# Performance work log

Hardware: AMD Instinct MI355X
Metric: run time of the kernel (lower is better)

The kernel has to match this reference:

```python
import jax, jax.numpy as jnp
import numpy as np

B, C, LQ, D = 4096, 64, 32, 128
H = 192  # 1.5 * dim
MARGIN = 1.0
EPS = 1e-12


def l2norm(x):
    return x * jax.lax.rsqrt(jnp.maximum(jnp.sum(x * x, axis=1, keepdims=True), EPS))


def setup_inputs() -> dict:
    key = jax.random.key(0)
    ks = jax.random.split(key, 16)
    question_word_embs = jax.random.normal(ks[0], (B, LQ, D), jnp.float32)
    question_lengths = jax.random.randint(ks[1], (B,), 1, LQ + 1, jnp.int32)
    header_embs = jax.random.normal(ks[2], (B, C, D), jnp.float32)
    table_word_embs = jax.random.normal(ks[3], (B, C, D), jnp.float32)
    num_cols = jax.random.randint(ks[4], (B,), 1, C + 1, jnp.int32)
    masks = (jnp.arange(C)[None, :] < num_cols[:, None]).astype(jnp.float32)
    labels = (jax.random.uniform(ks[5], (B,)) < 0.5).astype(jnp.float32)
    # table_encoder_dense: Dense(1.5*dim, relu) -> Dense(dim, relu)
    W1 = jax.random.normal(ks[6], (2 * D, H), jnp.float32) / np.sqrt(2 * D)
    b1 = jnp.zeros((H,), jnp.float32)
    W2 = jax.random.normal(ks[7], (H, D), jnp.float32) / np.sqrt(H)
    b2 = jnp.zeros((D,), jnp.float32)
    # query LSTM(dim, activation='relu'): gate order i, f, c, o (Keras)
    Wx = jax.random.normal(ks[8], (D, 4 * D), jnp.float32) / np.sqrt(D)
    Wh = jax.random.normal(ks[9], (D, 4 * D), jnp.float32) / np.sqrt(D)
    b_lstm = jnp.zeros((4 * D,), jnp.float32)
    return dict(question_word_embs=question_word_embs, question_lengths=question_lengths,
                header_embs=header_embs, table_word_embs=table_word_embs,
                num_cols=num_cols, masks=masks, labels=labels,
                W1=W1, b1=b1, W2=W2, b2=b2, Wx=Wx, Wh=Wh, b_lstm=b_lstm)


def masked_lstm(x, lengths, Wx, Wh, b):
    # x: [B, L, D]; returns final hidden state at each row's true length
    xs = jnp.transpose(x, (1, 0, 2))  # [L, B, D]
    h0 = jnp.zeros((x.shape[0], D), x.dtype)
    c0 = jnp.zeros_like(h0)

    def step(carry, inp):
        h, c = carry
        t, x_t = inp
        z = x_t @ Wx + h @ Wh + b  # [B, 4D]
        i, f, g, o = jnp.split(z, 4, axis=1)
        i = jax.nn.sigmoid(i)
        f = jax.nn.sigmoid(f)
        g = jax.nn.relu(g)           # activation='relu'
        o = jax.nn.sigmoid(o)
        c_new = f * c + i * g
        h_new = o * jax.nn.relu(c_new)
        m = (t < lengths)[:, None].astype(x_t.dtype)
        return (m * h_new + (1 - m) * h, m * c_new + (1 - m) * c), None

    (h, _), _ = jax.lax.scan(step, (h0, c0), (jnp.arange(xs.shape[0]), xs))
    return h


def reference(question_word_embs, question_lengths, header_embs, table_word_embs,
              num_cols, masks, labels, W1, b1, W2, b2, Wx, Wh, b_lstm):
    # ---- table path ----
    flat = jnp.concatenate([header_embs.reshape(-1, D), table_word_embs.reshape(-1, D)], axis=1)  # [B*C, 2D]
    h = jax.nn.relu(flat @ W1 + b1)
    te = jax.nn.relu(h @ W2 + b2).reshape(B, C, D)
    te = te * masks[:, :, None]
    te = jnp.sum(te, axis=1) / num_cols.astype(jnp.float32)[:, None]
    te = l2norm(te)
    # ---- query path (ragged-word LSTM encoder) ----
    qe = masked_lstm(question_word_embs, question_lengths, Wx, Wh, b_lstm)
    qe = l2norm(qe)
    # ---- contrastive loss ----
    d = jnp.sum(jnp.square(qe - te), axis=1)
    d_sqrt = jnp.sqrt(d)
    loss = labels * d + (1.0 - labels) * jnp.square(jnp.maximum(0.0, MARGIN - d_sqrt))
    return 0.5 * jnp.mean(loss)
```

## Files before the change

### kernel.cpp

```cpp
#include <hip/hip_runtime.h>
#include <math.h>

#define B_  4096
#define C_  64
#define LQ_ 32
#define D_  128
#define H_  192

typedef __attribute__((ext_vector_type(8))) short bf16x8;
typedef __attribute__((ext_vector_type(4))) float f32x4;

#define KEEP(x) asm volatile("" : "+v"(x))

__device__ inline unsigned cvt_pk_bf16(float lo, float hi) {
    unsigned r;
    asm("v_cvt_pk_bf16_f32 %0, %1, %2" : "=v"(r) : "v"(lo), "v"(hi));
    return r;
}
__device__ inline short f2b(float x) { return (short)(cvt_pk_bf16(x, x) & 0xffff); }
__device__ inline float sigm(float x) { return 1.f / (1.f + __expf(-x)); }

__device__ inline void wg_barrier() {
    asm volatile("s_waitcnt lgkmcnt(0)" ::: "memory");
    __builtin_amdgcn_s_barrier();
    asm volatile("" ::: "memory");
}
__device__ inline void wg_barrier_vm() {
    asm volatile("s_waitcnt vmcnt(0) lgkmcnt(0)" ::: "memory");
    __builtin_amdgcn_s_barrier();
    asm volatile("" ::: "memory");
}

__global__ __launch_bounds__(256) void prep_kernel(
    const float* __restrict__ W1, const float* __restrict__ W2,
    const float* __restrict__ Wx, const float* __restrict__ Wh,
    short* __restrict__ W1T, short* __restrict__ W2T, short* __restrict__ WTl)
{
    int idx = blockIdx.x * 256 + threadIdx.x;
    if (idx < 192 * 256) {
        int j = idx >> 8, k = idx & 255;
        W1T[idx] = f2b(W1[k * H_ + j]);
    }
    if (idx < 128 * 192) {
        int j = idx / 192, k = idx - j * 192;
        W2T[idx] = f2b(W2[k * D_ + j]);
    }
    if (idx < 512 * 256) {
        int p = idx >> 8, k = idx & 255;
        int w = p >> 6, g = (p >> 4) & 3, jj = p & 15;
        int jo = g * 128 + w * 16 + jj;
        float v = (k < 128) ? Wx[k * 512 + jo] : Wh[(k - 128) * 512 + jo];
        WTl[idx] = f2b(v);
    }
}

__global__ __launch_bounds__(256, 2)
void table_kernel(
    const float* __restrict__ header, const float* __restrict__ tword,
    const float* __restrict__ masks, const int* __restrict__ num_cols,
    const short* __restrict__ W1T, const float* __restrict__ b1,
    const short* __restrict__ W2T, const float* __restrict__ b2,
    float* __restrict__ te_out)
{
    const int bb0 = blockIdx.x * 4;
    const int tid = threadIdx.x;
    const int w   = tid >> 6;
    const int l   = tid & 63;
    const int lg  = l >> 4;
    const int ln  = l & 15;

    __shared__ __align__(16) float flat32[2][16 * 256];
    __shared__ __align__(16) short h_s[16 * 192];
    __shared__ float msk_s[4][64];
    __shared__ float ncol_s[4];
    __shared__ float redv[128];
    __shared__ float redq[2];

    bf16x8 bw1[3][8];
    float  bias1[3][4];
    #pragma unroll
    for (int ct = 0; ct < 3; ++ct) {
        int j = w * 48 + ct * 16 + ln;
        #pragma unroll
        for (int ks = 0; ks < 8; ++ks)
            bw1[ct][ks] = *(const bf16x8*)&W1T[j * 256 + ks * 32 + lg * 8];
        #pragma unroll
        for (int reg = 0; reg < 4; ++reg)
            bias1[ct][reg] = b1[w * 48 + ct * 16 + lg * 4 + reg];
    }
    #pragma unroll
    for (int ct = 0; ct < 3; ++ct) {
        #pragma unroll
        for (int ks = 0; ks < 8; ++ks) KEEP(bw1[ct][ks]);
        #pragma unroll
        for (int reg = 0; reg < 4; ++reg) KEEP(bias1[ct][reg]);
    }

    ((float*)msk_s)[tid] = masks[(size_t)bb0 * C_ + tid];
    if (tid < 4) ncol_s[tid] = (float)num_cols[bb0 + tid];

    auto stage_issue = [&](int cc, int buf) {
        int b    = bb0 + (cc >> 2);
        int row0 = (cc & 3) * 16;
        #pragma unroll
        for (int i = 0; i < 4; ++i) {
            int r = w * 4 + i;
            int p = ((l * 16) ^ ((r & 7) << 4)) >> 2;
            const float* srcp = (p < 128)
                ? header + ((size_t)b * C_ + row0 + r) * D_ + p
                : tword  + ((size_t)b * C_ + row0 + r) * D_ + (p - 128);
            __builtin_amdgcn_global_load_lds(
                (const __attribute__((address_space(1))) unsigned*)srcp,
                (__attribute__((address_space(3))) unsigned*)&flat32[buf][r * 256],
                16, 0, 0);
        }
    };

    stage_issue(0, 0);
    __syncthreads();

    float csum[2][4] = {{0.f, 0.f, 0.f, 0.f}, {0.f, 0.f, 0.f, 0.f}};
    const int swz = (ln & 7) << 4;

    for (int cc = 0; cc < 16; ++cc) {
        const int bi  = cc >> 2;
        const int cur = cc & 1;

        bf16x8 w2f[2][6];
        #pragma unroll
        for (int ct = 0; ct < 2; ++ct)
            #pragma unroll
            for (int ks = 0; ks < 6; ++ks)
                w2f[ct][ks] = *(const bf16x8*)&W2T[(w * 32 + ct * 16 + ln) * 192 + ks * 32 + lg * 8];
        float4 b2v[2];
        #pragma unroll
        for (int ct = 0; ct < 2; ++ct)
            b2v[ct] = *(const float4*)&b2[w * 32 + ct * 16 + lg * 4];
        if (cc + 1 < 16) stage_issue(cc + 1, cur ^ 1);

        {
            const char* fb = (const char*)flat32[cur] + ln * 1024;
            f32x4 acc[3];
            #pragma unroll
            for (int ct = 0; ct < 3; ++ct)
                acc[ct] = (f32x4){bias1[ct][0], bias1[ct][1], bias1[ct][2], bias1[ct][3]};
            #pragma unroll
            for (int ks = 0; ks < 8; ++ks) {
                int base = ks * 128 + lg * 32;
                f32x4 a0 = *(const f32x4*)(fb + ((base)      ^ swz));
                f32x4 a1 = *(const f32x4*)(fb + ((base + 16) ^ swz));
                unsigned uu[4];
                uu[0] = cvt_pk_bf16(a0[0], a0[1]);
                uu[1] = cvt_pk_bf16(a0[2], a0[3]);
                uu[2] = cvt_pk_bf16(a1[0], a1[1]);
                uu[3] = cvt_pk_bf16(a1[2], a1[3]);
                bf16x8 bfrag = *(bf16x8*)uu;
                #pragma unroll
                for (int ct = 0; ct < 3; ++ct)
                    acc[ct] = __builtin_amdgcn_mfma_f32_16x16x32_bf16(bw1[ct][ks], bfrag, acc[ct], 0, 0, 0);
            }
            #pragma unroll
            for (int ct = 0; ct < 3; ++ct) {
                int col0 = w * 48 + ct * 16 + lg * 4;
                uint2 hp;
                hp.x = cvt_pk_bf16(fmaxf(acc[ct][0], 0.f), fmaxf(acc[ct][1], 0.f));
                hp.y = cvt_pk_bf16(fmaxf(acc[ct][2], 0.f), fmaxf(acc[ct][3], 0.f));
                *(uint2*)((char*)h_s + ln * 384 + ((col0 * 2) ^ swz)) = hp;
            }
        }
        wg_barrier();

        {
            f32x4 acc2[2];
            #pragma unroll
            for (int ct = 0; ct < 2; ++ct)
                acc2[ct] = (f32x4){b2v[ct].x, b2v[ct].y, b2v[ct].z, b2v[ct].w};
            #pragma unroll
            for (int ks = 0; ks < 6; ++ks) {
                bf16x8 a = *(const bf16x8*)((char*)h_s + ln * 384 + ((ks * 64 + lg * 16) ^ swz));
                #pragma unroll
                for (int ct = 0; ct < 2; ++ct)
                    acc2[ct] = __builtin_amdgcn_mfma_f32_16x16x32_bf16(w2f[ct][ks], a, acc2[ct], 0, 0, 0);
            }
            float m = msk_s[bi][(cc & 3) * 16 + ln];
            #pragma unroll
            for (int ct = 0; ct < 2; ++ct)
                #pragma unroll
                for (int reg = 0; reg < 4; ++reg)
                    csum[ct][reg] = fmaf(fmaxf(acc2[ct][reg], 0.f), m, csum[ct][reg]);
        }

        if ((cc & 3) == 3) {
            #pragma unroll
            for (int s = 1; s < 16; s <<= 1)
                #pragma unroll
                for (int ct = 0; ct < 2; ++ct)
                    #pragma unroll
                    for (int reg = 0; reg < 4; ++reg)
                        csum[ct][reg] += __shfl_xor(csum[ct][reg], s, 64);
            if (ln == 0) {
                #pragma unroll
                for (int ct = 0; ct < 2; ++ct)
                    #pragma unroll
                    for (int reg = 0; reg < 4; ++reg)
                        redv[w * 32 + ct * 16 + lg * 4 + reg] = csum[ct][reg];
            }
            wg_barrier();
            float v = 0.f;
            if (tid < 128) {
                v = redv[tid] / ncol_s[bi];
                float s2 = v * v;
                #pragma unroll
                for (int sh = 1; sh < 64; sh <<= 1) s2 += __shfl_xor(s2, sh, 64);
                if (l == 0) redq[w] = s2;
            }
            wg_barrier();
            if (tid < 128) {
                float inv = rsqrtf(fmaxf(redq[0] + redq[1], 1e-12f));
                te_out[(size_t)(bb0 + bi) * D_ + tid] = v * inv;
            }
            #pragma unroll
            for (int ct = 0; ct < 2; ++ct)
                #pragma unroll
                for (int reg = 0; reg < 4; ++reg)
                    csum[ct][reg] = 0.f;
        }

        wg_barrier_vm();
    }
}

__global__ __launch_bounds__(512) __attribute__((amdgpu_waves_per_eu(1, 2)))
void lstm_kernel(
    const float* __restrict__ q, const int* __restrict__ lengths,
    const short* __restrict__ WTl, const float* __restrict__ bl,
    float* __restrict__ qe_out)
{
    const int tid = threadIdx.x;
    const int b0  = blockIdx.x * 16;
    const int w   = tid >> 6;
    const int l   = tid & 63;
    const int lg  = l >> 4;
    const int ln  = l & 15;
    const int d0  = w * 16 + lg * 4;

    __shared__ __align__(16) short xh[2][16 * 256];
    __shared__ float red8[8][16];

    bf16x8 wf[4][8];
    #pragma unroll
    for (int g = 0; g < 4; ++g)
        #pragma unroll
        for (int ks = 0; ks < 8; ++ks)
            wf[g][ks] = *(const bf16x8*)&WTl[(w * 64 + g * 16 + ln) * 256 + ks * 32 + lg * 8];
    float bias[4][4];
    #pragma unroll
    for (int g = 0; g < 4; ++g)
        #pragma unroll
        for (int reg = 0; reg < 4; ++reg)
            bias[g][reg] = bl[g * 128 + d0 + reg];
    #pragma unroll
    for (int g = 0; g < 4; ++g) {
        #pragma unroll
        for (int ks = 0; ks < 8; ++ks) KEEP(wf[g][ks]);
        #pragma unroll
        for (int reg = 0; reg < 4; ++reg) KEEP(bias[g][reg]);
    }

    float creg[4] = {0.f, 0.f, 0.f, 0.f};
    float hreg[4] = {0.f, 0.f, 0.f, 0.f};
    const int len = lengths[b0 + ln];
    const int sr = tid >> 5, sc = tid & 31;

    float4 qv = *(const float4*)&q[((size_t)(b0 + sr) * LQ_ + 0) * D_ + sc * 4];

    for (int t = 0; t < LQ_; ++t) {
        char* buf = (char*)xh[t & 1];
        uint2 px; px.x = cvt_pk_bf16(qv.x, qv.y); px.y = cvt_pk_bf16(qv.z, qv.w);
        *(uint2*)(buf + sr * 512 + ((sc * 8) ^ ((sr & 7) << 4))) = px;
        uint2 ph; ph.x = cvt_pk_bf16(hreg[0], hreg[1]); ph.y = cvt_pk_bf16(hreg[2], hreg[3]);
        *(uint2*)(buf + ln * 512 + ((256 + d0 * 2) ^ ((ln & 7) << 4))) = ph;
        if (t + 1 < LQ_)
            qv = *(const float4*)&q[((size_t)(b0 + sr) * LQ_ + (t + 1)) * D_ + sc * 4];
        wg_barrier();

        f32x4 acc[4];
        #pragma unroll
        for (int g = 0; g < 4; ++g)
            acc[g] = (f32x4){bias[g][0], bias[g][1], bias[g][2], bias[g][3]};
        #pragma unroll
        for (int ks = 0; ks < 8; ++ks) {
            bf16x8 xf = *(const bf16x8*)(buf + ln * 512 + ((ks * 64 + lg * 16) ^ ((ln & 7) << 4)));
            #pragma unroll
            for (int g = 0; g < 4; ++g)
                acc[g] = __builtin_amdgcn_mfma_f32_16x16x32_bf16(wf[g][ks], xf, acc[g], 0, 0, 0);
        }

        bool live = (t < len);
        #pragma unroll
        for (int reg = 0; reg < 4; ++reg) {
            float iv = sigm(acc[0][reg]);
            float fv = sigm(acc[1][reg]);
            float gv = fmaxf(acc[2][reg], 0.f);
            float ov = sigm(acc[3][reg]);
            float cn = fmaf(fv, creg[reg], iv * gv);
            float hn = ov * fmaxf(cn, 0.f);
            if (live) { creg[reg] = cn; hreg[reg] = hn; }
        }
    }

    float sq = 0.f;
    #pragma unroll
    for (int reg = 0; reg < 4; ++reg) sq = fmaf(hreg[reg], hreg[reg], sq);
    sq += __shfl_xor(sq, 16, 64);
    sq += __shfl_xor(sq, 32, 64);
    if (l < 16) red8[w][ln] = sq;
    wg_barrier();
    float tot = 0.f;
    #pragma unroll
    for (int ww = 0; ww < 8; ++ww) tot += red8[ww][ln];
    float inv = rsqrtf(fmaxf(tot, 1e-12f));
    float4 o;
    o.x = hreg[0] * inv; o.y = hreg[1] * inv; o.z = hreg[2] * inv; o.w = hreg[3] * inv;
    *(float4*)&qe_out[(size_t)(b0 + ln) * D_ + d0] = o;
}

__global__ __launch_bounds__(64) void loss_kernel(
    const float* __restrict__ te, const float* __restrict__ qe,
    const float* __restrict__ labels, float* __restrict__ partial)
{
    const int tid = threadIdx.x;
    const int b   = blockIdx.x * 64 + tid;
    float dsum = 0.f;
    #pragma unroll 8
    for (int k4 = 0; k4 < 32; ++k4) {
        float4 a = *(const float4*)&qe[(size_t)b * D_ + k4 * 4];
        float4 c = *(const float4*)&te[(size_t)b * D_ + k4 * 4];
        float dx = a.x - c.x, dy = a.y - c.y, dz = a.z - c.z, dw = a.w - c.w;
        dsum += dx * dx + dy * dy + dz * dz + dw * dw;
    }
    float lab = labels[b];
    float ds  = sqrtf(dsum);
    float ml  = fmaxf(0.f, 1.f - ds);
    float loss = lab * dsum + (1.f - lab) * ml * ml;
    #pragma unroll
    for (int s = 32; s > 0; s >>= 1) loss += __shfl_xor(loss, s, 64);
    if (tid == 0) partial[blockIdx.x] = loss;
}

__global__ void final_kernel(const float* __restrict__ partial, float* __restrict__ out)
{
    const int tid = threadIdx.x;
    float v = partial[tid];
    #pragma unroll
    for (int s = 32; s > 0; s >>= 1) v += __shfl_xor(v, s, 64);
    if (tid == 0) out[0] = 0.5f * v / (float)B_;
}

extern "C" void kernel_launch(void* const* d_in, const int* in_sizes, int n_in,
                              void* d_out, int out_size, void* d_ws, size_t ws_size,
                              hipStream_t stream)
{
    const float* q      = (const float*)d_in[0];
    const int*   qlen   = (const int*)d_in[1];
    const float* header = (const float*)d_in[2];
    const float* tword  = (const float*)d_in[3];
    const int*   ncols  = (const int*)d_in[4];
    const float* masks  = (const float*)d_in[5];
    const float* labels = (const float*)d_in[6];
    const float* W1     = (const float*)d_in[7];
    const float* b1     = (const float*)d_in[8];
    const float* W2     = (const float*)d_in[9];
    const float* b2     = (const float*)d_in[10];
    const float* Wx     = (const float*)d_in[11];
    const float* Wh     = (const float*)d_in[12];
    const float* bl     = (const float*)d_in[13];
    float* out = (float*)d_out;

    float* te      = (float*)d_ws;
    float* qe      = te + (size_t)B_ * D_;
    float* partial = qe + (size_t)B_ * D_;
    short* W1T     = (short*)(partial + 64);
    short* W2T     = W1T + 192 * 256;
    short* WTl     = W2T + 128 * 192;

    prep_kernel<<<512, 256, 0, stream>>>(W1, W2, Wx, Wh, W1T, W2T, WTl);
    table_kernel<<<B_ / 4, 256, 0, stream>>>(header, tword, masks, ncols, W1T, b1, W2T, b2, te);
    lstm_kernel<<<B_ / 16, 512, 0, stream>>>(q, qlen, WTl, bl, qe);
    loss_kernel<<<B_ / 64, 64, 0, stream>>>(te, qe, labels, partial);
    final_kernel<<<1, 64, 0, stream>>>(partial, out);
}
```

Baseline: 166.8 us.

## Triple-buffer table staging and defer per-batch normalization to kernel end

The table kernel now keeps three LDS staging buffers and prefetches two chunks ahead. The per-iteration barrier waits only until the older async global-to-LDS loads are done (vmcnt(4)) instead of draining all of them. The per-batch mean/L2-norm reduction, which used two extra barriers every four chunks, now happens once at the end using per-batch shared sums. This costs more LDS per block and adds a barrier reached by only two of the four waves, which depends on finished waves not blocking it.

```diff
diff --git a/kernel.cpp b/kernel.cpp
--- a/kernel.cpp
+++ b/kernel.cpp
@@ -22,11 +22,6 @@
 
 __device__ inline void wg_barrier() {
     asm volatile("s_waitcnt lgkmcnt(0)" ::: "memory");
-    __builtin_amdgcn_s_barrier();
-    asm volatile("" ::: "memory");
-}
-__device__ inline void wg_barrier_vm() {
-    asm volatile("s_waitcnt vmcnt(0) lgkmcnt(0)" ::: "memory");
     __builtin_amdgcn_s_barrier();
     asm volatile("" ::: "memory");
 }
@@ -69,12 +64,12 @@
     const int lg  = l >> 4;
     const int ln  = l & 15;
 
-    __shared__ __align__(16) float flat32[2][16 * 256];
+    __shared__ __align__(16) float flat32[3][16 * 256];
     __shared__ __align__(16) short h_s[16 * 192];
     __shared__ float msk_s[4][64];
     __shared__ float ncol_s[4];
-    __shared__ float redv[128];
-    __shared__ float redq[2];
+    __shared__ float csum_s[4][128];
+    __shared__ float redq[2][4];
 
     bf16x8 bw1[3][8];
     float  bias1[3][4];
@@ -117,14 +112,15 @@
     };
 
     stage_issue(0, 0);
+    stage_issue(1, 1);
     __syncthreads();
 
     float csum[2][4] = {{0.f, 0.f, 0.f, 0.f}, {0.f, 0.f, 0.f, 0.f}};
     const int swz = (ln & 7) << 4;
 
+    #pragma unroll 1
     for (int cc = 0; cc < 16; ++cc) {
-        const int bi  = cc >> 2;
-        const int cur = cc & 1;
+        const int bi = cc >> 2;
 
         bf16x8 w2f[2][6];
         #pragma unroll
@@ -136,10 +132,10 @@
         #pragma unroll
         for (int ct = 0; ct < 2; ++ct)
             b2v[ct] = *(const float4*)&b2[w * 32 + ct * 16 + lg * 4];
-        if (cc + 1 < 16) stage_issue(cc + 1, cur ^ 1);
+        if (cc + 2 < 16) stage_issue(cc + 2, (cc + 2) % 3);
 
         {
-            const char* fb = (const char*)flat32[cur] + ln * 1024;
+            const char* fb = (const char*)flat32[cc % 3] + ln * 1024;
             f32x4 acc[3];
             #pragma unroll
             for (int ct = 0; ct < 3; ++ct)
@@ -203,21 +199,7 @@
                 for (int ct = 0; ct < 2; ++ct)
                     #pragma unroll
                     for (int reg = 0; reg < 4; ++reg)
-                        redv[w * 32 + ct * 16 + lg * 4 + reg] = csum[ct][reg];
-            }
-            wg_barrier();
-            float v = 0.f;
-            if (tid < 128) {
-                v = redv[tid] / ncol_s[bi];
-                float s2 = v * v;
-                #pragma unroll
-                for (int sh = 1; sh < 64; sh <<= 1) s2 += __shfl_xor(s2, sh, 64);
-                if (l == 0) redq[w] = s2;
-            }
-            wg_barrier();
-            if (tid < 128) {
-                float inv = rsqrtf(fmaxf(redq[0] + redq[1], 1e-12f));
-                te_out[(size_t)(bb0 + bi) * D_ + tid] = v * inv;
+                        csum_s[bi][w * 32 + ct * 16 + lg * 4 + reg] = csum[ct][reg];
             }
             #pragma unroll
             for (int ct = 0; ct < 2; ++ct)
@@ -226,7 +208,35 @@
                     csum[ct][reg] = 0.f;
         }
 
-        wg_barrier_vm();
+        if (cc < 14) {
+            asm volatile("s_waitcnt vmcnt(4) lgkmcnt(0)" ::: "memory");
+            __builtin_amdgcn_s_barrier();
+            asm volatile("" ::: "memory");
+        } else if (cc == 14) {
+            asm volatile("s_waitcnt vmcnt(0) lgkmcnt(0)" ::: "memory");
+            __builtin_amdgcn_s_barrier();
+            asm volatile("" ::: "memory");
+        }
+    }
+
+    __syncthreads();
+    if (tid < 128) {
+        float vv[4];
+        #pragma unroll
+        for (int bi = 0; bi < 4; ++bi) {
+            float v = csum_s[bi][tid] / ncol_s[bi];
+            vv[bi] = v;
+            float s2 = v * v;
+            #pragma unroll
+            for (int sh = 1; sh < 64; sh <<= 1) s2 += __shfl_xor(s2, sh, 64);
+            if (l == 0) redq[w][bi] = s2;
+        }
+        __builtin_amdgcn_s_barrier();
+        #pragma unroll
+        for (int bi = 0; bi < 4; ++bi) {
+            float inv = rsqrtf(fmaxf(redq[0][bi] + redq[1][bi], 1e-12f));
+            te_out[(size_t)(bb0 + bi) * D_ + tid] = vv[bi] * inv;
+        }
     }
 }
 
```

After: 152.5 us. 8.6% less time.
